# Kernel tuning notes

Measured on AMD Instinct MI355X. Metric: run time of the kernel, lower is better.

## Reference

```python
import jax, jax.numpy as jnp
import numpy as np

KH = KW = 9
STRIDE = 1
PAD = 4
DIL = 1


def _bilinear(img, py, px):
    """img: [C,H,W]; py, px: [kk,Ho,Wo] float sample coords -> [C,kk,Ho,Wo].
    Zero padding outside the image, matching DCNv2 semantics."""
    H, W = img.shape[-2], img.shape[-1]
    y0 = jnp.floor(py)
    x0 = jnp.floor(px)
    wy = py - y0  # fractional parts (carry the gradient wrt offsets)
    wx = px - x0

    def gather(yi, xi):
        valid = ((yi >= 0) & (yi < H) & (xi >= 0) & (xi < W)).astype(img.dtype)
        yc = jnp.clip(yi, 0, H - 1).astype(jnp.int32)
        xc = jnp.clip(xi, 0, W - 1).astype(jnp.int32)
        return img[:, yc, xc] * valid[None]

    v00 = gather(y0, x0)
    v01 = gather(y0, x0 + 1)
    v10 = gather(y0 + 1, x0)
    v11 = gather(y0 + 1, x0 + 1)
    return (v00 * (1 - wy) * (1 - wx) + v01 * (1 - wy) * wx
            + v10 * wy * (1 - wx) + v11 * wy * wx)


def setup_inputs() -> dict:
    key = jax.random.key(0)
    k1, k2, k3 = jax.random.split(key, 3)
    B, H, W = 2, 256, 256
    kk = KH * KW
    inp = jax.random.normal(k1, (B, 3, H, W), dtype=jnp.float32)
    offset = jax.random.normal(k2, (B, 2 * kk, H, W), dtype=jnp.float32)
    mask = jax.random.uniform(k3, (B, kk, H, W), dtype=jnp.float32)
    weight = jnp.ones((1, 1, KH, KW), dtype=jnp.float32) / kk  # frozen averaging kernel
    bias = jnp.zeros((1,), dtype=jnp.float32)
    return {"input": inp, "offset": offset, "mask": mask, "weight": weight, "bias": bias}


def reference(input, offset, mask, weight, bias):
    B, C, H, W = input.shape  # C = 3 * Ci (R,G,B chunks sharing weight/offset/mask)
    kk = KH * KW
    Ho = (H + 2 * PAD - DIL * (KH - 1) - 1) // STRIDE + 1
    Wo = (W + 2 * PAD - DIL * (KW - 1) - 1) // STRIDE + 1

    ky = jnp.repeat(jnp.arange(KH), KW)  # [kk]
    kx = jnp.tile(jnp.arange(KW), KH)
    base_y = (jnp.arange(Ho) * STRIDE - PAD)[None, :, None] + (ky * DIL)[:, None, None]  # [kk,Ho,1]
    base_x = (jnp.arange(Wo) * STRIDE - PAD)[None, None, :] + (kx * DIL)[:, None, None]  # [kk,1,Wo]

    off = offset.reshape(B, kk, 2, Ho, Wo)  # channel c = 2*k + {0: dy, 1: dx}
    py = base_y[None].astype(offset.dtype) + off[:, :, 0]  # [B,kk,Ho,Wo]
    px = base_x[None].astype(offset.dtype) + off[:, :, 1]

    # bilinear-sampled, modulated im2col: [B, C, kk, Ho, Wo]
    samples = jax.vmap(_bilinear)(input, py, px)
    val = samples * mask[:, None]

    Co, Ci = weight.shape[0], weight.shape[1]
    G = C // Ci  # 3 color groups, identical weight applied to each
    val = val.reshape(B, G, Ci, kk, Ho, Wo)
    wk = weight.reshape(Co, Ci, kk)
    out = jnp.einsum('bgckhw,ock->bgohw', val, wk) + bias[None, None, :, None, None]
    return out.reshape(B, G * Co, Ho, Wo)
```

## Files before the change

### kernel.cpp

```cpp
#include <hip/hip_runtime.h>
#include <hip/hip_fp16.h>

#define HH 256
#define WW 256
#define KK 81
#define PLANE (HH * WW)
#define SLACK 10
#define TR 21
#define TC 84
#define TAB (TR * TC)

__global__ __launch_bounds__(256) void pack_kernel(const float* __restrict__ in,
                                                   ushort4* __restrict__ img) {
    int idx = blockIdx.x * 256 + threadIdx.x;
    int b = idx >> 16;
    int pix = idx & 0xFFFF;
    const float* base = in + (size_t)b * 3 * PLANE + pix;
    _Float16 h0 = (_Float16)base[0];
    _Float16 h1 = (_Float16)base[PLANE];
    _Float16 h2 = (_Float16)base[2 * PLANE];
    ushort4 u;
    u.x = __builtin_bit_cast(unsigned short, h0);
    u.y = __builtin_bit_cast(unsigned short, h1);
    u.z = __builtin_bit_cast(unsigned short, h2);
    u.w = 0;
    img[idx] = u;
}

__device__ __forceinline__ void acc3(float w, unsigned int pa, unsigned int pb,
                                     float& ax, float& ay, float& az) {
    __half2 ha = __builtin_bit_cast(__half2, pa);
    __half2 hb = __builtin_bit_cast(__half2, pb);
    ax = fmaf(w, __low2float(ha), ax);
    ay = fmaf(w, __high2float(ha), ay);
    az = fmaf(w, __low2float(hb), az);
}

__global__ __launch_bounds__(256, 4) void dcn_kernel(
    const ushort4* __restrict__ img,
    const float* __restrict__ offset,
    const float* __restrict__ mask,
    const float* __restrict__ weight,
    const float* __restrict__ bias,
    float* __restrict__ out) {
    __shared__ uint2 tile[TAB];
    __shared__ float red[3][4][64];

    const int t = threadIdx.x;
    const int b = blockIdx.y;
    const int pix0 = blockIdx.x * 64;
    const int ho = pix0 >> 8;
    const int xb = (pix0 & 255) - SLACK;
    const int yb = ho - SLACK;
    const ushort4* ib = img + (size_t)b * PLANE;

    const int w = t >> 6;
    const int lane = t & 63;
    const int pix = pix0 + lane;
    const int kbeg = w * 20;

    const float* op = offset + (size_t)b * 2 * KK * PLANE + (size_t)(2 * kbeg) * PLANE + pix;
    const float* mp = mask + (size_t)b * KK * PLANE + (size_t)kbeg * PLANE + pix;

    float pdy[21], pdx[21], pm[21];
#pragma unroll
    for (int j = 0; j < 21; ++j) {
        pdy[j] = op[(size_t)(2 * j) * PLANE];
        pdx[j] = op[(size_t)(2 * j + 1) * PLANE];
        pm[j] = mp[(size_t)j * PLANE] * weight[kbeg + j];
    }

    for (int i = 0; i < 7; ++i) {
        int cid = t + i * 256;
        if (cid < TAB) {
            int r = cid / TC;
            int c = cid - r * TC;
            int iy = yb + r;
            int ix = xb + c;
            unsigned int pa = 0, pb = 0;
            if (((unsigned)iy < (unsigned)HH) & ((unsigned)ix < (unsigned)WW)) {
                ushort4 u = ib[iy * WW + ix];
                pa = (unsigned int)u.x | ((unsigned int)u.y << 16);
                pb = (unsigned int)u.z;
            }
            tile[cid] = make_uint2(pa, pb);
        }
    }

    __syncthreads();

    const float wof = (float)((pix0 & 255) + lane);
    float ax = 0.f, ay = 0.f, az = 0.f;
    unsigned int fail = 0u;
    int ky = 2 * w;
    int kx = 2 * w;

#pragma unroll
    for (int j = 0; j < 21; ++j) {
        float m = pm[j];
        if (w != 0 && j == 0) m = 0.f;

        float py = (float)(ho - 4 + ky) + pdy[j];
        float px = wof + ((float)(kx - 4) + pdx[j]);
        float y0f = floorf(py), x0f = floorf(px);
        float wy = py - y0f, wx = px - x0f;
        int r0 = (int)y0f - yb;
        int c0 = (int)x0f - xb;

        bool ok = ((unsigned)r0 < (TR - 1)) & ((unsigned)c0 < (TC - 1));
        fail |= (ok ? 0u : 1u) << j;
        m = ok ? m : 0.f;

        float w1y = wy * m, w0y = m - w1y;
        float w00 = w0y * (1.f - wx), w01 = w0y * wx;
        float w10 = w1y * (1.f - wx), w11 = w1y * wx;

        int r0c = min(max(r0, 0), TR - 2);
        int c0c = min(max(c0, 0), TC - 2);
        const uint2* p = &tile[r0c * TC + c0c];
        uint2 q00 = p[0];
        uint2 q01 = p[1];
        uint2 q10 = p[TC];
        uint2 q11 = p[TC + 1];

        acc3(w00, q00.x, q00.y, ax, ay, az);
        acc3(w01, q01.x, q01.y, ax, ay, az);
        acc3(w10, q10.x, q10.y, ax, ay, az);
        acc3(w11, q11.x, q11.y, ax, ay, az);

        if (++kx == 9) {
            kx = 0;
            ++ky;
        }
    }

    if (__builtin_expect(fail != 0u, 0)) {
        while (fail) {
            int j = __ffs(fail) - 1;
            fail &= fail - 1;
            if (w != 0 && j == 0) continue;
            int k = kbeg + j;
            float dy = op[(size_t)(2 * j) * PLANE];
            float dx = op[(size_t)(2 * j + 1) * PLANE];
            float m = mp[(size_t)j * PLANE] * weight[k];
            int kyy = k / 9;
            int kxx = k - kyy * 9;
            float py = (float)(ho - 4 + kyy) + dy;
            float px = wof + ((float)(kxx - 4) + dx);
            float y0f = floorf(py), x0f = floorf(px);
            float wy = py - y0f, wx = px - x0f;
            int y0 = (int)y0f, x0 = (int)x0f;
            int y1 = y0 + 1, x1 = x0 + 1;
            float va0 = ((unsigned)y0 < (unsigned)HH) ? 1.f : 0.f;
            float va1 = ((unsigned)y1 < (unsigned)HH) ? 1.f : 0.f;
            float vb0 = ((unsigned)x0 < (unsigned)WW) ? 1.f : 0.f;
            float vb1 = ((unsigned)x1 < (unsigned)WW) ? 1.f : 0.f;
            float w1y = wy * m, w0y = m - w1y;
            float w00 = w0y * (1.f - wx) * va0 * vb0;
            float w01 = w0y * wx * va0 * vb1;
            float w10 = w1y * (1.f - wx) * va1 * vb0;
            float w11 = w1y * wx * va1 * vb1;
            int y0c = min(max(y0, 0), HH - 1);
            int y1c = min(max(y1, 0), HH - 1);
            int x0c = min(max(x0, 0), WW - 1);
            int x1c = min(max(x1, 0), WW - 1);
            ushort4 g00 = ib[y0c * WW + x0c];
            ushort4 g01 = ib[y0c * WW + x1c];
            ushort4 g10 = ib[y1c * WW + x0c];
            ushort4 g11 = ib[y1c * WW + x1c];
            acc3(w00, (unsigned int)g00.x | ((unsigned int)g00.y << 16), g00.z, ax, ay, az);
            acc3(w01, (unsigned int)g01.x | ((unsigned int)g01.y << 16), g01.z, ax, ay, az);
            acc3(w10, (unsigned int)g10.x | ((unsigned int)g10.y << 16), g10.z, ax, ay, az);
            acc3(w11, (unsigned int)g11.x | ((unsigned int)g11.y << 16), g11.z, ax, ay, az);
        }
    }

    red[0][w][lane] = ax;
    red[1][w][lane] = ay;
    red[2][w][lane] = az;
    __syncthreads();

    if (t < 192) {
        const int c = t >> 6;
        const int l = t & 63;
        float s = red[c][0][l] + red[c][1][l] + red[c][2][l] + red[c][3][l] + bias[0];
        out[(size_t)b * 3 * PLANE + (size_t)c * PLANE + pix0 + l] = s;
    }
}

extern "C" void kernel_launch(void* const* d_in, const int* in_sizes, int n_in,
                              void* d_out, int out_size, void* d_ws, size_t ws_size,
                              hipStream_t stream) {
    const float* input = (const float*)d_in[0];
    const float* offset = (const float*)d_in[1];
    const float* mask = (const float*)d_in[2];
    const float* weight = (const float*)d_in[3];
    const float* bias = (const float*)d_in[4];
    float* out = (float*)d_out;

    const int B = in_sizes[0] / (3 * PLANE);
    ushort4* img = (ushort4*)d_ws;

    pack_kernel<<<B * PLANE / 256, 256, 0, stream>>>(input, img);
    dim3 grid(PLANE / 64, B);
    dcn_kernel<<<grid, 256, 0, stream>>>(img, offset, mask, weight, bias, out);
}
```

Measured before the change: 180.8 us.

## Process full output rows per block with double-buffered async offset/mask loads to LDS

Each block now handles one full 256-pixel output row, with each thread owning one pixel and looping over all 81 taps. It stages a 17x272 halo tile of the packed image in LDS. Offsets and mask are streamed in chunks of four taps with global_load_lds into a double buffer, so the next chunk's fetch overlaps compute on the current one. This removes the cross-wave reduction and the large per-thread register arrays. The cost is a larger halo tile per block (extra LDS loading), a __syncthreads per chunk, and occupancy lowered to 2 blocks per SIMD.

```diff
diff --git a/kernel.cpp b/kernel.cpp
--- a/kernel.cpp
+++ b/kernel.cpp
@@ -5,10 +5,12 @@
 #define WW 256
 #define KK 81
 #define PLANE (HH * WW)
-#define SLACK 10
-#define TR 21
-#define TC 84
-#define TAB (TR * TC)
+#define TR 17
+#define TC2 272
+#define XB (-8)
+#define YOFF 8
+#define CT 4
+#define NCH 21
 
 __global__ __launch_bounds__(256) void pack_kernel(const float* __restrict__ in,
                                                    ushort4* __restrict__ img) {
@@ -36,47 +38,50 @@
     az = fmaf(w, __low2float(hb), az);
 }
 
-__global__ __launch_bounds__(256, 4) void dcn_kernel(
+__device__ __forceinline__ void gload_lds16(const float* g, float* l) {
+    __builtin_amdgcn_global_load_lds(
+        (const __attribute__((address_space(1))) unsigned int*)g,
+        (__attribute__((address_space(3))) unsigned int*)l,
+        16, 0, 0);
+}
+
+__global__ __launch_bounds__(256, 2) void dcn_kernel(
     const ushort4* __restrict__ img,
     const float* __restrict__ offset,
     const float* __restrict__ mask,
     const float* __restrict__ weight,
     const float* __restrict__ bias,
     float* __restrict__ out) {
-    __shared__ uint2 tile[TAB];
-    __shared__ float red[3][4][64];
+    __shared__ uint2 tile[TR * TC2];
+    __shared__ float cbuf[2][CT][3][256];
 
     const int t = threadIdx.x;
-    const int b = blockIdx.y;
-    const int pix0 = blockIdx.x * 64;
-    const int ho = pix0 >> 8;
-    const int xb = (pix0 & 255) - SLACK;
-    const int yb = ho - SLACK;
-    const ushort4* ib = img + (size_t)b * PLANE;
-
     const int w = t >> 6;
     const int lane = t & 63;
-    const int pix = pix0 + lane;
-    const int kbeg = w * 20;
-
-    const float* op = offset + (size_t)b * 2 * KK * PLANE + (size_t)(2 * kbeg) * PLANE + pix;
-    const float* mp = mask + (size_t)b * KK * PLANE + (size_t)kbeg * PLANE + pix;
-
-    float pdy[21], pdx[21], pm[21];
-#pragma unroll
-    for (int j = 0; j < 21; ++j) {
-        pdy[j] = op[(size_t)(2 * j) * PLANE];
-        pdx[j] = op[(size_t)(2 * j + 1) * PLANE];
-        pm[j] = mp[(size_t)j * PLANE] * weight[kbeg + j];
+    const int b = blockIdx.y;
+    const int ho = blockIdx.x;
+    const int yb = ho - YOFF;
+    const ushort4* ib = img + (size_t)b * PLANE;
+
+    const float* orow = offset + (size_t)b * 2 * KK * PLANE + (size_t)ho * WW;
+    const float* mrow = mask + (size_t)b * KK * PLANE + (size_t)ho * WW;
+
+    {
+        int k = w;
+        float* dst = &cbuf[0][w][0][0];
+        const float* gdy = orow + (size_t)(2 * k) * PLANE + lane * 4;
+        gload_lds16(gdy, dst);
+        gload_lds16(gdy + PLANE, dst + 256);
+        gload_lds16(mrow + (size_t)k * PLANE + lane * 4, dst + 512);
     }
 
-    for (int i = 0; i < 7; ++i) {
+    for (int i = 0; i < 19; ++i) {
         int cid = t + i * 256;
-        if (cid < TAB) {
-            int r = cid / TC;
-            int c = cid - r * TC;
+        if (cid < TR * TC2) {
+            int r = cid / TC2;
+            int c = cid - r * TC2;
             int iy = yb + r;
-            int ix = xb + c;
+            int ix = XB + c;
             unsigned int pa = 0, pb = 0;
             if (((unsigned)iy < (unsigned)HH) & ((unsigned)ix < (unsigned)WW)) {
                 ushort4 u = ib[iy * WW + ix];
@@ -86,106 +91,113 @@
             tile[cid] = make_uint2(pa, pb);
         }
     }
-
     __syncthreads();
 
-    const float wof = (float)((pix0 & 255) + lane);
+    const float wof = (float)t;
     float ax = 0.f, ay = 0.f, az = 0.f;
-    unsigned int fail = 0u;
-    int ky = 2 * w;
-    int kx = 2 * w;
+
+    for (int c = 0; c < NCH; ++c) {
+        {
+            int k = (c + 1) * CT + w;
+            if (k < KK) {
+                float* dst = &cbuf[(c + 1) & 1][w][0][0];
+                const float* gdy = orow + (size_t)(2 * k) * PLANE + lane * 4;
+                gload_lds16(gdy, dst);
+                gload_lds16(gdy + PLANE, dst + 256);
+                gload_lds16(mrow + (size_t)k * PLANE + lane * 4, dst + 512);
+            }
+        }
+
+        const int cur = c & 1;
+        unsigned int fl = 0;
 
 #pragma unroll
-    for (int j = 0; j < 21; ++j) {
-        float m = pm[j];
-        if (w != 0 && j == 0) m = 0.f;
-
-        float py = (float)(ho - 4 + ky) + pdy[j];
-        float px = wof + ((float)(kx - 4) + pdx[j]);
-        float y0f = floorf(py), x0f = floorf(px);
-        float wy = py - y0f, wx = px - x0f;
-        int r0 = (int)y0f - yb;
-        int c0 = (int)x0f - xb;
-
-        bool ok = ((unsigned)r0 < (TR - 1)) & ((unsigned)c0 < (TC - 1));
-        fail |= (ok ? 0u : 1u) << j;
-        m = ok ? m : 0.f;
-
-        float w1y = wy * m, w0y = m - w1y;
-        float w00 = w0y * (1.f - wx), w01 = w0y * wx;
-        float w10 = w1y * (1.f - wx), w11 = w1y * wx;
-
-        int r0c = min(max(r0, 0), TR - 2);
-        int c0c = min(max(c0, 0), TC - 2);
-        const uint2* p = &tile[r0c * TC + c0c];
-        uint2 q00 = p[0];
-        uint2 q01 = p[1];
-        uint2 q10 = p[TC];
-        uint2 q11 = p[TC + 1];
-
-        acc3(w00, q00.x, q00.y, ax, ay, az);
-        acc3(w01, q01.x, q01.y, ax, ay, az);
-        acc3(w10, q10.x, q10.y, ax, ay, az);
-        acc3(w11, q11.x, q11.y, ax, ay, az);
-
-        if (++kx == 9) {
-            kx = 0;
-            ++ky;
-        }
+        for (int tc = 0; tc < CT; ++tc) {
+            int k = c * CT + tc;
+            if (k < KK) {
+                const float* cb = &cbuf[cur][tc][0][0];
+                float dy = cb[t];
+                float dx = cb[256 + t];
+                float m = cb[512 + t] * weight[k];
+                int ky = k / 9, kx = k - ky * 9;
+                float py = (float)(ho - 4 + ky) + dy;
+                float px = wof + ((float)(kx - 4) + dx);
+                float y0f = floorf(py), x0f = floorf(px);
+                float wy = py - y0f, wx = px - x0f;
+                int r0 = (int)y0f - yb;
+                int c0 = (int)x0f - XB;
+
+                bool ok = ((unsigned)r0 < (TR - 1)) & ((unsigned)c0 < (TC2 - 1));
+                fl |= (ok ? 0u : 1u) << tc;
+                m = ok ? m : 0.f;
+
+                float w1y = wy * m, w0y = m - w1y;
+                float w00 = w0y * (1.f - wx), w01 = w0y * wx;
+                float w10 = w1y * (1.f - wx), w11 = w1y * wx;
+
+                int r0c = min(max(r0, 0), TR - 2);
+                int c0c = min(max(c0, 0), TC2 - 2);
+                const uint2* p = &tile[r0c * TC2 + c0c];
+                uint2 q00 = p[0];
+                uint2 q01 = p[1];
+                uint2 q10 = p[TC2];
+                uint2 q11 = p[TC2 + 1];
+
+                acc3(w00, q00.x, q00.y, ax, ay, az);
+                acc3(w01, q01.x, q01.y, ax, ay, az);
+                acc3(w10, q10.x, q10.y, ax, ay, az);
+                acc3(w11, q11.x, q11.y, ax, ay, az);
+            }
+        }
+
+        if (__builtin_expect(fl != 0u, 0)) {
+            while (fl) {
+                int tc = __ffs(fl) - 1;
+                fl &= fl - 1;
+                int k = c * CT + tc;
+                const float* cb = &cbuf[cur][0][0][0] + tc * 768;
+                float dy = cb[t];
+                float dx = cb[256 + t];
+                float m = cb[512 + t] * weight[k];
+                int ky = k / 9, kx = k - ky * 9;
+                float py = (float)(ho - 4 + ky) + dy;
+                float px = wof + ((float)(kx - 4) + dx);
+                float y0f = floorf(py), x0f = floorf(px);
+                float wy = py - y0f, wx = px - x0f;
+                int y0 = (int)y0f, x0 = (int)x0f;
+                int y1 = y0 + 1, x1 = x0 + 1;
+                float va0 = ((unsigned)y0 < (unsigned)HH) ? 1.f : 0.f;
+                float va1 = ((unsigned)y1 < (unsigned)HH) ? 1.f : 0.f;
+                float vb0 = ((unsigned)x0 < (unsigned)WW) ? 1.f : 0.f;
+                float vb1 = ((unsigned)x1 < (unsigned)WW) ? 1.f : 0.f;
+                float w1y = wy * m, w0y = m - w1y;
+                float w00 = w0y * (1.f - wx) * va0 * vb0;
+                float w01 = w0y * wx * va0 * vb1;
+                float w10 = w1y * (1.f - wx) * va1 * vb0;
+                float w11 = w1y * wx * va1 * vb1;
+                int y0c = min(max(y0, 0), HH - 1);
+                int y1c = min(max(y1, 0), HH - 1);
+                int x0c = min(max(x0, 0), WW - 1);
+                int x1c = min(max(x1, 0), WW - 1);
+                ushort4 g00 = ib[y0c * WW + x0c];
+                ushort4 g01 = ib[y0c * WW + x1c];
+                ushort4 g10 = ib[y1c * WW + x0c];
+                ushort4 g11 = ib[y1c * WW + x1c];
+                acc3(w00, (unsigned int)g00.x | ((unsigned int)g00.y << 16), g00.z, ax, ay, az);
+                acc3(w01, (unsigned int)g01.x | ((unsigned int)g01.y << 16), g01.z, ax, ay, az);
+                acc3(w10, (unsigned int)g10.x | ((unsigned int)g10.y << 16), g10.z, ax, ay, az);
+                acc3(w11, (unsigned int)g11.x | ((unsigned int)g11.y << 16), g11.z, ax, ay, az);
+            }
+        }
+
+        __syncthreads();
     }
 
-    if (__builtin_expect(fail != 0u, 0)) {
-        while (fail) {
-            int j = __ffs(fail) - 1;
-            fail &= fail - 1;
-            if (w != 0 && j == 0) continue;
-            int k = kbeg + j;
-            float dy = op[(size_t)(2 * j) * PLANE];
-            float dx = op[(size_t)(2 * j + 1) * PLANE];
-            float m = mp[(size_t)j * PLANE] * weight[k];
-            int kyy = k / 9;
-            int kxx = k - kyy * 9;
-            float py = (float)(ho - 4 + kyy) + dy;
-            float px = wof + ((float)(kxx - 4) + dx);
-            float y0f = floorf(py), x0f = floorf(px);
-            float wy = py - y0f, wx = px - x0f;
-            int y0 = (int)y0f, x0 = (int)x0f;
-            int y1 = y0 + 1, x1 = x0 + 1;
-            float va0 = ((unsigned)y0 < (unsigned)HH) ? 1.f : 0.f;
-            float va1 = ((unsigned)y1 < (unsigned)HH) ? 1.f : 0.f;
-            float vb0 = ((unsigned)x0 < (unsigned)WW) ? 1.f : 0.f;
-            float vb1 = ((unsigned)x1 < (unsigned)WW) ? 1.f : 0.f;
-            float w1y = wy * m, w0y = m - w1y;
-            float w00 = w0y * (1.f - wx) * va0 * vb0;
-            float w01 = w0y * wx * va0 * vb1;
-            float w10 = w1y * (1.f - wx) * va1 * vb0;
-            float w11 = w1y * wx * va1 * vb1;
-            int y0c = min(max(y0, 0), HH - 1);
-            int y1c = min(max(y1, 0), HH - 1);
-            int x0c = min(max(x0, 0), WW - 1);
-            int x1c = min(max(x1, 0), WW - 1);
-            ushort4 g00 = ib[y0c * WW + x0c];
-            ushort4 g01 = ib[y0c * WW + x1c];
-            ushort4 g10 = ib[y1c * WW + x0c];
-            ushort4 g11 = ib[y1c * WW + x1c];
-            acc3(w00, (unsigned int)g00.x | ((unsigned int)g00.y << 16), g00.z, ax, ay, az);
-            acc3(w01, (unsigned int)g01.x | ((unsigned int)g01.y << 16), g01.z, ax, ay, az);
-            acc3(w10, (unsigned int)g10.x | ((unsigned int)g10.y << 16), g10.z, ax, ay, az);
-            acc3(w11, (unsigned int)g11.x | ((unsigned int)g11.y << 16), g11.z, ax, ay, az);
-        }
-    }
-
-    red[0][w][lane] = ax;
-    red[1][w][lane] = ay;
-    red[2][w][lane] = az;
-    __syncthreads();
-
-    if (t < 192) {
-        const int c = t >> 6;
-        const int l = t & 63;
-        float s = red[c][0][l] + red[c][1][l] + red[c][2][l] + red[c][3][l] + bias[0];
-        out[(size_t)b * 3 * PLANE + (size_t)c * PLANE + pix0 + l] = s;
-    }
+    float bs = bias[0];
+    float* ob = out + (size_t)b * 3 * PLANE + (size_t)ho * WW + t;
+    ob[0] = ax + bs;
+    ob[PLANE] = ay + bs;
+    ob[2 * PLANE] = az + bs;
 }
 
 extern "C" void kernel_launch(void* const* d_in, const int* in_sizes, int n_in,
@@ -202,6 +214,6 @@
     ushort4* img = (ushort4*)d_ws;
 
     pack_kernel<<<B * PLANE / 256, 256, 0, stream>>>(input, img);
-    dim3 grid(PLANE / 64, B);
+    dim3 grid(HH, B);
     dcn_kernel<<<grid, 256, 0, stream>>>(img, offset, mask, weight, bias, out);
 }
```

Measured after the change: 170.5 us. 5.7% less time.

## Give each thread all 81 taps over a 128-pixel half-row tile

Applied to the files above, without the earlier changes.

The work is remapped from four waves each handling a fifth of the taps for 64 pixels to one thread per pixel handling all 81 taps, with 128-thread blocks covering half a row. This removes the shared-memory cross-wave reduction and its extra barrier, and each thread writes its output directly. The shared tile is widened to 150 columns, so each block stages a larger image region and fewer blocks fit per CU. Offset and mask loads are now issued inside the tap loop rather than prefetched into registers, which lowers register pressure but may expose load latency.

```diff
diff --git a/kernel.cpp b/kernel.cpp
--- a/kernel.cpp
+++ b/kernel.cpp
@@ -5,9 +5,9 @@
 #define WW 256
 #define KK 81
 #define PLANE (HH * WW)
-#define SLACK 10
+#define SLK 10
 #define TR 21
-#define TC 84
+#define TC 150
 #define TAB (TR * TC)
 
 __global__ __launch_bounds__(256) void pack_kernel(const float* __restrict__ in,
@@ -36,7 +36,7 @@
     az = fmaf(w, __low2float(hb), az);
 }
 
-__global__ __launch_bounds__(256, 4) void dcn_kernel(
+__global__ __launch_bounds__(128, 3) void dcn_kernel(
     const ushort4* __restrict__ img,
     const float* __restrict__ offset,
     const float* __restrict__ mask,
@@ -44,39 +44,21 @@
     const float* __restrict__ bias,
     float* __restrict__ out) {
     __shared__ uint2 tile[TAB];
-    __shared__ float red[3][4][64];
 
     const int t = threadIdx.x;
     const int b = blockIdx.y;
-    const int pix0 = blockIdx.x * 64;
-    const int ho = pix0 >> 8;
-    const int xb = (pix0 & 255) - SLACK;
-    const int yb = ho - SLACK;
+    const int ho = blockIdx.x >> 1;
+    const int xo = (blockIdx.x & 1) * 128;
+    const int yb = ho - SLK;
     const ushort4* ib = img + (size_t)b * PLANE;
 
-    const int w = t >> 6;
-    const int lane = t & 63;
-    const int pix = pix0 + lane;
-    const int kbeg = w * 20;
-
-    const float* op = offset + (size_t)b * 2 * KK * PLANE + (size_t)(2 * kbeg) * PLANE + pix;
-    const float* mp = mask + (size_t)b * KK * PLANE + (size_t)kbeg * PLANE + pix;
-
-    float pdy[21], pdx[21], pm[21];
-#pragma unroll
-    for (int j = 0; j < 21; ++j) {
-        pdy[j] = op[(size_t)(2 * j) * PLANE];
-        pdx[j] = op[(size_t)(2 * j + 1) * PLANE];
-        pm[j] = mp[(size_t)j * PLANE] * weight[kbeg + j];
-    }
-
-    for (int i = 0; i < 7; ++i) {
-        int cid = t + i * 256;
+    for (int i = 0; i < 25; ++i) {
+        int cid = t + i * 128;
         if (cid < TAB) {
             int r = cid / TC;
             int c = cid - r * TC;
             int iy = yb + r;
-            int ix = xb + c;
+            int ix = xo - SLK + c;
             unsigned int pa = 0, pb = 0;
             if (((unsigned)iy < (unsigned)HH) & ((unsigned)ix < (unsigned)WW)) {
                 ushort4 u = ib[iy * WW + ix];
@@ -86,76 +68,88 @@
             tile[cid] = make_uint2(pa, pb);
         }
     }
-
     __syncthreads();
 
-    const float wof = (float)((pix0 & 255) + lane);
+    const float* orow = offset + (size_t)b * 2 * KK * PLANE + (size_t)ho * WW + xo;
+    const float* mrow = mask + (size_t)b * KK * PLANE + (size_t)ho * WW + xo;
+
+    const float wof = (float)t;
     float ax = 0.f, ay = 0.f, az = 0.f;
-    unsigned int fail = 0u;
-    int ky = 2 * w;
-    int kx = 2 * w;
+    bool escaped = false;
 
+    for (int ky = 0; ky < 9; ++ky) {
+        const int rshift = ky + (SLK - 4);
 #pragma unroll
-    for (int j = 0; j < 21; ++j) {
-        float m = pm[j];
-        if (w != 0 && j == 0) m = 0.f;
+        for (int kxi = 0; kxi < 9; ++kxi) {
+            const int k = ky * 9 + kxi;
+            float dy = orow[(size_t)(2 * k) * PLANE + t];
+            float dx = orow[(size_t)(2 * k + 1) * PLANE + t];
+            float m = mrow[(size_t)k * PLANE + t];
+            float wk = weight[k];
 
-        float py = (float)(ho - 4 + ky) + pdy[j];
-        float px = wof + ((float)(kx - 4) + pdx[j]);
-        float y0f = floorf(py), x0f = floorf(px);
-        float wy = py - y0f, wx = px - x0f;
-        int r0 = (int)y0f - yb;
-        int c0 = (int)x0f - xb;
+            float yf = floorf(dy);
+            float wy = dy - yf;
+            int r0 = (int)yf + rshift;
 
-        bool ok = ((unsigned)r0 < (TR - 1)) & ((unsigned)c0 < (TC - 1));
-        fail |= (ok ? 0u : 1u) << j;
-        m = ok ? m : 0.f;
+            float px = dx + wof;
+            float xf = floorf(px);
+            float wx = px - xf;
+            int c0 = (int)xf + (kxi + (SLK - 4));
 
-        float w1y = wy * m, w0y = m - w1y;
-        float w00 = w0y * (1.f - wx), w01 = w0y * wx;
-        float w10 = w1y * (1.f - wx), w11 = w1y * wx;
+            bool ok = ((unsigned)r0 < (unsigned)(TR - 1)) &
+                      ((unsigned)c0 < (unsigned)(TC - 1));
+            escaped |= !ok;
+            float mw = (ok ? m : 0.f) * wk;
 
-        int r0c = min(max(r0, 0), TR - 2);
-        int c0c = min(max(c0, 0), TC - 2);
-        const uint2* p = &tile[r0c * TC + c0c];
-        uint2 q00 = p[0];
-        uint2 q01 = p[1];
-        uint2 q10 = p[TC];
-        uint2 q11 = p[TC + 1];
+            float w1y = wy * mw, w0y = mw - w1y;
+            float u1 = 1.f - wx;
+            float w00 = w0y * u1, w01 = w0y * wx;
+            float w10 = w1y * u1, w11 = w1y * wx;
 
-        acc3(w00, q00.x, q00.y, ax, ay, az);
-        acc3(w01, q01.x, q01.y, ax, ay, az);
-        acc3(w10, q10.x, q10.y, ax, ay, az);
-        acc3(w11, q11.x, q11.y, ax, ay, az);
+            int r0c = min(max(r0, 0), TR - 2);
+            int c0c = min(max(c0, 0), TC - 2);
+            const uint2* p = &tile[r0c * TC + c0c];
+            uint2 q00 = p[0];
+            uint2 q01 = p[1];
+            uint2 q10 = p[TC];
+            uint2 q11 = p[TC + 1];
 
-        if (++kx == 9) {
-            kx = 0;
-            ++ky;
+            acc3(w00, q00.x, q00.y, ax, ay, az);
+            acc3(w01, q01.x, q01.y, ax, ay, az);
+            acc3(w10, q10.x, q10.y, ax, ay, az);
+            acc3(w11, q11.x, q11.y, ax, ay, az);
         }
     }
 
-    if (__builtin_expect(fail != 0u, 0)) {
-        while (fail) {
-            int j = __ffs(fail) - 1;
-            fail &= fail - 1;
-            if (w != 0 && j == 0) continue;
-            int k = kbeg + j;
-            float dy = op[(size_t)(2 * j) * PLANE];
-            float dx = op[(size_t)(2 * j + 1) * PLANE];
-            float m = mp[(size_t)j * PLANE] * weight[k];
-            int kyy = k / 9;
-            int kxx = k - kyy * 9;
-            float py = (float)(ho - 4 + kyy) + dy;
-            float px = wof + ((float)(kxx - 4) + dx);
-            float y0f = floorf(py), x0f = floorf(px);
-            float wy = py - y0f, wx = px - x0f;
-            int y0 = (int)y0f, x0 = (int)x0f;
+    if (__builtin_expect(escaped, 0)) {
+#pragma unroll 1
+        for (int k = 0; k < KK; ++k) {
+            int ky = k / 9;
+            int kxi = k - ky * 9;
+            float dy = orow[(size_t)(2 * k) * PLANE + t];
+            float dx = orow[(size_t)(2 * k + 1) * PLANE + t];
+            float m = mrow[(size_t)k * PLANE + t];
+
+            float yf = floorf(dy);
+            int r0 = (int)yf + ky + (SLK - 4);
+            float px = dx + wof;
+            float xf = floorf(px);
+            int c0 = (int)xf + kxi + (SLK - 4);
+            bool ok = ((unsigned)r0 < (unsigned)(TR - 1)) &
+                      ((unsigned)c0 < (unsigned)(TC - 1));
+            if (ok) continue;
+
+            float wy = dy - yf;
+            float wx = px - xf;
+            int y0 = (int)yf + ho - 4 + ky;
+            int x0 = (int)xf + xo + kxi - 4;
             int y1 = y0 + 1, x1 = x0 + 1;
+            float mw = m * weight[k];
             float va0 = ((unsigned)y0 < (unsigned)HH) ? 1.f : 0.f;
             float va1 = ((unsigned)y1 < (unsigned)HH) ? 1.f : 0.f;
             float vb0 = ((unsigned)x0 < (unsigned)WW) ? 1.f : 0.f;
             float vb1 = ((unsigned)x1 < (unsigned)WW) ? 1.f : 0.f;
-            float w1y = wy * m, w0y = m - w1y;
+            float w1y = wy * mw, w0y = mw - w1y;
             float w00 = w0y * (1.f - wx) * va0 * vb0;
             float w01 = w0y * wx * va0 * vb1;
             float w10 = w1y * (1.f - wx) * va1 * vb0;
@@ -175,17 +169,11 @@
         }
     }
 
-    red[0][w][lane] = ax;
-    red[1][w][lane] = ay;
-    red[2][w][lane] = az;
-    __syncthreads();
-
-    if (t < 192) {
-        const int c = t >> 6;
-        const int l = t & 63;
-        float s = red[c][0][l] + red[c][1][l] + red[c][2][l] + red[c][3][l] + bias[0];
-        out[(size_t)b * 3 * PLANE + (size_t)c * PLANE + pix0 + l] = s;
-    }
+    float bs = bias[0];
+    float* ob = out + (size_t)b * 3 * PLANE + (size_t)ho * WW + xo + t;
+    ob[0] = ax + bs;
+    ob[PLANE] = ay + bs;
+    ob[2 * PLANE] = az + bs;
 }
 
 extern "C" void kernel_launch(void* const* d_in, const int* in_sizes, int n_in,
@@ -202,6 +190,6 @@
     ushort4* img = (ushort4*)d_ws;
 
     pack_kernel<<<B * PLANE / 256, 256, 0, stream>>>(input, img);
-    dim3 grid(PLANE / 64, B);
-    dcn_kernel<<<grid, 256, 0, stream>>>(img, offset, mask, weight, bias, out);
+    dim3 grid(HH * 2, B);
+    dcn_kernel<<<grid, 128, 0, stream>>>(img, offset, mask, weight, bias, out);
 }
```

Measured after the change: 172.8 us. 1.05x faster.
